# Optimization experiments

Measured on AMD Instinct MI355X. Metric: run time of the kernel, lower is better.

## Reference

```python
import jax, jax.numpy as jnp
import numpy as np

DIM = 768
HEADS = 12
HIDDEN = 3072  # int(dim * 4.0)
EPS = 1e-5


def layernorm(x, g, b):
    mu = jnp.mean(x, axis=-1, keepdims=True)
    var = jnp.mean(jnp.square(x - mu), axis=-1, keepdims=True)
    return (x - mu) * jax.lax.rsqrt(var + EPS) * g + b


def setup_inputs() -> dict:
    key = jax.random.key(0)
    ks = jax.random.split(key, 8)
    s = 0.02
    return {
        "x": jax.random.normal(ks[0], (16, 1024, DIM), dtype=jnp.float32),
        "ln1_g": jnp.ones((DIM,), jnp.float32),
        "ln1_b": jnp.zeros((DIM,), jnp.float32),
        "qkv_w": jax.random.normal(ks[1], (3 * DIM, DIM), jnp.float32) * s,  # torch Linear weight [out,in], no bias (qkv_bias=False)
        "proj_w": jax.random.normal(ks[2], (DIM, DIM), jnp.float32) * s,
        "proj_b": jnp.zeros((DIM,), jnp.float32),
        "ln2_g": jnp.ones((DIM,), jnp.float32),
        "ln2_b": jnp.zeros((DIM,), jnp.float32),
        "fc1_w": jax.random.normal(ks[3], (HIDDEN, DIM), jnp.float32) * s,
        "fc1_b": jnp.zeros((HIDDEN,), jnp.float32),
        "fc2_w": jax.random.normal(ks[4], (DIM, HIDDEN), jnp.float32) * s,
        "fc2_b": jnp.zeros((DIM,), jnp.float32),
    }


def block(x, ln1_g, ln1_b, qkv_w, proj_w, proj_b, ln2_g, ln2_b, fc1_w, fc1_b, fc2_w, fc2_b):
    B, N, C = x.shape
    hd = C // HEADS
    scale = hd ** -0.5
    # --- attention branch ---
    h = layernorm(x, ln1_g, ln1_b)
    qkv = h @ qkv_w.T                                   # [B,N,3C]
    qkv = qkv.reshape(B, N, 3, HEADS, hd)
    q, k, v = jnp.moveaxis(qkv, 2, 0)                   # each [B,N,H,hd]
    q = q.transpose(0, 2, 1, 3)                          # [B,H,N,hd]
    k = k.transpose(0, 2, 1, 3)
    v = v.transpose(0, 2, 1, 3)
    attn = jnp.einsum('bhqd,bhkd->bhqk', q, k) * scale   # [B,H,N,N]
    attn = jax.nn.softmax(attn, axis=-1)
    o = jnp.einsum('bhqk,bhkd->bhqd', attn, v)           # [B,H,N,hd]
    o = o.transpose(0, 2, 1, 3).reshape(B, N, C)
    x = x + o @ proj_w.T + proj_b
    # --- mlp branch ---
    h = layernorm(x, ln2_g, ln2_b)
    h = jax.nn.gelu(h @ fc1_w.T + fc1_b, approximate=False)
    x = x + h @ fc2_w.T + fc2_b
    return x


def reference(x, ln1_g, ln1_b, qkv_w, proj_w, proj_b, ln2_g, ln2_b, fc1_w, fc1_b, fc2_w, fc2_b):
    return block(x, ln1_g, ln1_b, qkv_w, proj_w, proj_b, ln2_g, ln2_b, fc1_w, fc1_b, fc2_w, fc2_b)
```

## Files before the change

kernel.cpp:

```cpp
#include <hip/hip_runtime.h>
#include <cstdint>
#include <cstddef>

typedef __attribute__((ext_vector_type(8))) short short8;
typedef __attribute__((ext_vector_type(4))) float f32x4;
typedef __attribute__((ext_vector_type(4))) unsigned short us4;

#define GAS(p) ((const __attribute__((address_space(1))) void*)(p))
#define LAS(p) ((__attribute__((address_space(3))) void*)(p))

__device__ __forceinline__ unsigned short f2bf(float f) {
  union { float f; unsigned u; } v; v.f = f;
  return (unsigned short)((v.u + 0x7fffu + ((v.u >> 16) & 1u)) >> 16);
}

__global__ __launch_bounds__(256) void cvt_kernel(const float* __restrict__ in,
                                                  unsigned short* __restrict__ out, int n4) {
  int i = blockIdx.x * 256 + threadIdx.x;
  if (i >= n4) return;
  f32x4 v = ((const f32x4*)in)[i];
  us4 o;
#pragma unroll
  for (int j = 0; j < 4; ++j) o[j] = f2bf(v[j]);
  ((us4*)out)[i] = o;
}

__global__ __launch_bounds__(256) void ln_kernel(const float* __restrict__ x,
                                                 const float* __restrict__ g,
                                                 const float* __restrict__ b,
                                                 unsigned short* __restrict__ out) {
  const int wave = threadIdx.x >> 6, lane = threadIdx.x & 63;
  const int row = blockIdx.x * 4 + wave;
  const float* xr = x + (size_t)row * 768;
  f32x4 v[3];
  float s = 0.f, sq = 0.f;
#pragma unroll
  for (int c = 0; c < 3; ++c) {
    v[c] = *(const f32x4*)(xr + c * 256 + lane * 4);
#pragma unroll
    for (int j = 0; j < 4; ++j) { s += v[c][j]; sq += v[c][j] * v[c][j]; }
  }
#pragma unroll
  for (int off = 32; off > 0; off >>= 1) { s += __shfl_xor(s, off); sq += __shfl_xor(sq, off); }
  const float mu = s * (1.f / 768.f);
  const float var = sq * (1.f / 768.f) - mu * mu;
  const float rs = rsqrtf(var + 1e-5f);
  unsigned short* orow = out + (size_t)row * 768;
#pragma unroll
  for (int c = 0; c < 3; ++c) {
    f32x4 gg = *(const f32x4*)(g + c * 256 + lane * 4);
    f32x4 bb = *(const f32x4*)(b + c * 256 + lane * 4);
    us4 o;
#pragma unroll
    for (int j = 0; j < 4; ++j) o[j] = f2bf((v[c][j] - mu) * rs * gg[j] + bb[j]);
    *(us4*)(orow + c * 256 + lane * 4) = o;
  }
}

template <int EPI, int NN, int K>
__global__ __launch_bounds__(1024, 4) void gemmW(
    const unsigned short* __restrict__ A, const unsigned short* __restrict__ W,
    float* __restrict__ outF, const float* __restrict__ bias, const float* __restrict__ res,
    unsigned short* __restrict__ outU,
    unsigned short* __restrict__ q, unsigned short* __restrict__ kk, unsigned short* __restrict__ vt) {
  __shared__ unsigned short As[4][8192];
  __shared__ unsigned short Bs[4][8192];
  const int tid = threadIdx.x;
  const int wave = tid >> 6, lane = tid & 63;
  const int lr = lane & 15, lg = lane >> 4;
  const int wr = wave >> 2, wc = wave & 3;
  constexpr int GX = NN / 256;
  constexpr int NWG = GX * 64;
  int id = blockIdx.y * GX + blockIdx.x;
  id = (id & 7) * (NWG / 8) + (id >> 3);
  const int row0 = (id / GX) * 256, col0 = (id % GX) * 256;
  f32x4 acc[4][4] = {};
  const int sc = ((tid & 3) ^ ((tid >> 3) & 3)) * 8;
  const unsigned short* ag = A + (size_t)(row0 + (tid >> 2)) * K + sc;
  const unsigned short* bg = W + (size_t)(col0 + (tid >> 2)) * K + sc;
  const int rsw = (lg ^ ((lr >> 1) & 3)) << 4;
  constexpr int KT = K / 32;

#define STG(buf, t_)                                                                           \
  {                                                                                            \
    __builtin_amdgcn_global_load_lds(GAS(ag + (t_) * 32), LAS(&As[buf][wave * 512]), 16, 0, 0);\
    __builtin_amdgcn_global_load_lds(GAS(bg + (t_) * 32), LAS(&Bs[buf][wave * 512]), 16, 0, 0);\
  }

#define TILE(buf, t_)                                                                          \
  {                                                                                            \
    if ((t_) < KT - 2)       { asm volatile("s_waitcnt vmcnt(4)" ::: "memory"); }              \
    else if ((t_) == KT - 2) { asm volatile("s_waitcnt vmcnt(2)" ::: "memory"); }              \
    else                     { asm volatile("s_waitcnt vmcnt(0)" ::: "memory"); }              \
    __builtin_amdgcn_s_barrier();                                                              \
    if ((t_) + 3 < KT) STG(((buf) + 3) & 3, (t_) + 3);                                         \
    const char* Ab = (const char*)As + (buf) * 16384;                                          \
    const char* Bb = (const char*)Bs + (buf) * 16384;                                          \
    short8 af[4], bfv[4];                                                                      \
    _Pragma("unroll")                                                                          \
    for (int m = 0; m < 4; ++m) {                                                              \
      const int arow = wr * 64 + m * 16 + lr;                                                  \
      af[m] = *(const short8*)(Ab + arow * 64 + rsw);                                          \
    }                                                                                          \
    _Pragma("unroll")                                                                          \
    for (int n = 0; n < 4; ++n) {                                                              \
      const int brow = wc * 64 + n * 16 + lr;                                                  \
      bfv[n] = *(const short8*)(Bb + brow * 64 + rsw);                                         \
    }                                                                                          \
    __builtin_amdgcn_s_setprio(1);                                                             \
    _Pragma("unroll")                                                                          \
    for (int m = 0; m < 4; ++m)                                                                \
      _Pragma("unroll")                                                                        \
      for (int n = 0; n < 4; ++n)                                                              \
        acc[m][n] = __builtin_amdgcn_mfma_f32_16x16x32_bf16(af[m], bfv[n], acc[m][n], 0, 0, 0);\
    __builtin_amdgcn_s_setprio(0);                                                             \
  }

  STG(0, 0);
  STG(1, 1);
  STG(2, 2);
  for (int tt = 0; tt < KT; tt += 4) {
    TILE(0, tt);
    TILE(1, tt + 1);
    TILE(2, tt + 2);
    TILE(3, tt + 3);
  }
#undef TILE
#undef STG

  if (EPI == 0) {
    const int s = (col0 >= 1536) ? 2 : (col0 >= 768 ? 1 : 0);
    const int hh = (col0 + wc * 64 - s * 768) >> 6;
#pragma unroll
    for (int m = 0; m < 4; ++m)
#pragma unroll
      for (int n = 0; n < 4; ++n) {
        const int d = n * 16 + lr;
        const int g0 = row0 + wr * 64 + m * 16 + lg * 4;
        const int bt = g0 >> 10, nt0 = g0 & 1023;
        const size_t bh = (size_t)(bt * 12 + hh);
        if (s == 2) {
          us4 o;
#pragma unroll
          for (int r = 0; r < 4; ++r) o[r] = f2bf(acc[m][n][r]);
          *(us4*)(vt + (bh * 64 + d) * 1024 + nt0) = o;
        } else {
#pragma unroll
          for (int r = 0; r < 4; ++r) {
            const float val = acc[m][n][r];
            if (s == 0) q[(bh * 1024 + nt0 + r) * 64 + d] = f2bf(val * 0.125f);
            else        kk[(bh * 1024 + nt0 + r) * 64 + d] = f2bf(val);
          }
        }
      }
  } else if (EPI == 1) {
#pragma unroll
    for (int m = 0; m < 4; ++m)
#pragma unroll
      for (int n = 0; n < 4; ++n) {
        const int gcol = col0 + wc * 64 + n * 16 + lr;
        const float bn = bias[gcol];
#pragma unroll
        for (int r = 0; r < 4; ++r) {
          const int grow = row0 + wr * 64 + m * 16 + lg * 4 + r;
          const size_t idx = (size_t)grow * NN + gcol;
          outF[idx] = acc[m][n][r] + bn + res[idx];
        }
      }
  } else {
#pragma unroll
    for (int m = 0; m < 4; ++m)
#pragma unroll
      for (int n = 0; n < 4; ++n) {
        const int gcol = col0 + wc * 64 + n * 16 + lr;
        const float bn = bias[gcol];
#pragma unroll
        for (int r = 0; r < 4; ++r) {
          const int grow = row0 + wr * 64 + m * 16 + lg * 4 + r;
          const size_t idx = (size_t)grow * NN + gcol;
          const float t = acc[m][n][r] + bn;
          const float u = t * (1.59576912f + t * t * 0.07135481f);
          const float eu = __expf(-u);
          outU[idx] = f2bf(t / (1.f + eu));
        }
      }
  }
}

__global__ __launch_bounds__(256) void attn_kernel(
    const unsigned short* __restrict__ Q, const unsigned short* __restrict__ K,
    const unsigned short* __restrict__ V, unsigned short* __restrict__ O) {
  __shared__ unsigned short Ks[2][64 * 64];
  __shared__ unsigned short Vs[2][64 * 64];
  const int tid = threadIdx.x, wave = tid >> 6, lane = tid & 63;
  const int lr = lane & 15, lg = lane >> 4;
  const int id = blockIdx.x;
  const int qt = (id >> 3) & 7;
  const int head = (id & 7) + 8 * (id >> 6);
  const int hh = head % 12, bb = head / 12;
  const size_t bh = (size_t)bb * 12 + hh;
  const unsigned short* Qg = Q + bh * 1024 * 64;
  const unsigned short* Kg = K + bh * 1024 * 64;
  const unsigned short* Vg = V + bh * 64 * 1024;
  const int q0 = qt * 128 + wave * 32;
  short8 aq[2][2];
#pragma unroll
  for (int nq = 0; nq < 2; ++nq)
#pragma unroll
    for (int kb = 0; kb < 2; ++kb)
      aq[nq][kb] = *(const short8*)(Qg + (size_t)(q0 + nq * 16 + lr) * 64 + kb * 32 + lg * 8);
  float m_run[2] = {-1e30f, -1e30f}, l_run[2] = {0.f, 0.f};
  f32x4 oacc[4][2] = {};
  const int srow = tid >> 3;
  const int sswz = (((tid & 7) * 16) ^ ((srow & 7) << 4)) >> 1;
  const int srcLo = (lane & 15) | ((lane & 16) << 1);
  const int srcHi = srcLo + 16;
  const bool hiSel = lg >= 2;

#define ATTN_STAGE(buf, t_)                                                                      \
  {                                                                                              \
    const int kv_ = (t_) * 64;                                                                   \
    _Pragma("unroll")                                                                            \
    for (int is = 0; is < 2; ++is) {                                                             \
      __builtin_amdgcn_global_load_lds(GAS(Kg + (size_t)(kv_ + is * 32 + srow) * 64 + sswz),     \
                                       LAS(&Ks[buf][is * 2048 + wave * 512]), 16, 0, 0);         \
      __builtin_amdgcn_global_load_lds(GAS(Vg + (size_t)(is * 32 + srow) * 1024 + kv_ + sswz),   \
                                       LAS(&Vs[buf][is * 2048 + wave * 512]), 16, 0, 0);         \
    }                                                                                            \
  }

#define ATILE(cur, t_)                                                                           \
  {                                                                                              \
    if ((t_) < 15) { asm volatile("s_waitcnt vmcnt(4)" ::: "memory"); }                          \
    else           { asm volatile("s_waitcnt vmcnt(0)" ::: "memory"); }                          \
    __builtin_amdgcn_s_barrier();                                                                \
    __builtin_amdgcn_sched_barrier(0);                                                           \
    f32x4 sacc[4][2] = {};                                                                       \
    _Pragma("unroll")                                                                            \
    for (int kb = 0; kb < 2; ++kb) {                                                             \
      short8 kf[4];                                                                              \
      _Pragma("unroll")                                                                          \
      for (int mk = 0; mk < 4; ++mk) {                                                           \
        const int row = mk * 16 + lr;                                                            \
        const int boff = row * 128 + ((kb * 64 + lg * 16) ^ ((row & 7) << 4));                   \
        kf[mk] = *(const short8*)((const char*)&Ks[cur][0] + boff);                              \
      }                                                                                          \
      _Pragma("unroll")                                                                          \
      for (int mk = 0; mk < 4; ++mk)                                                             \
        _Pragma("unroll")                                                                        \
        for (int nq = 0; nq < 2; ++nq)                                                           \
          sacc[mk][nq] = __builtin_amdgcn_mfma_f32_16x16x32_bf16(kf[mk], aq[nq][kb], sacc[mk][nq], 0, 0, 0); \
    }                                                                                            \
    unsigned pk[4][2][2];                                                                        \
    _Pragma("unroll")                                                                            \
    for (int nq = 0; nq < 2; ++nq) {                                                             \
      float mx = fmaxf(fmaxf(sacc[0][nq][0], sacc[0][nq][1]), fmaxf(sacc[0][nq][2], sacc[0][nq][3])); \
      _Pragma("unroll")                                                                          \
      for (int mk = 1; mk < 4; ++mk)                                                             \
        mx = fmaxf(mx, fmaxf(fmaxf(sacc[mk][nq][0], sacc[mk][nq][1]), fmaxf(sacc[mk][nq][2], sacc[mk][nq][3]))); \
      mx = fmaxf(mx, __shfl_xor(mx, 16));                                                        \
      mx = fmaxf(mx, __shfl_xor(mx, 32));                                                        \
      if (!__all(mx - m_run[nq] <= 8.f)) {                                                       \
        const float mnew = fmaxf(m_run[nq], mx);                                                 \
        const float alpha = __expf(m_run[nq] - mnew);                                            \
        l_run[nq] *= alpha;                                                                      \
        _Pragma("unroll")                                                                        \
        for (int mb = 0; mb < 4; ++mb)                                                           \
          _Pragma("unroll")                                                                      \
          for (int r = 0; r < 4; ++r) oacc[mb][nq][r] *= alpha;                                  \
        m_run[nq] = mnew;                                                                        \
      }                                                                                          \
      float ssum = 0.f;                                                                          \
      _Pragma("unroll")                                                                          \
      for (int mk = 0; mk < 4; ++mk)                                                             \
        _Pragma("unroll")                                                                        \
        for (int r = 0; r < 4; ++r) {                                                            \
          const float p = __expf(sacc[mk][nq][r] - m_run[nq]);                                   \
          sacc[mk][nq][r] = p;                                                                   \
          ssum += p;                                                                             \
        }                                                                                        \
      ssum += __shfl_xor(ssum, 16);                                                              \
      ssum += __shfl_xor(ssum, 32);                                                              \
      l_run[nq] += ssum;                                                                         \
      _Pragma("unroll")                                                                          \
      for (int mk = 0; mk < 4; ++mk) {                                                           \
        asm("v_cvt_pk_bf16_f32 %0, %1, %2" : "=v"(pk[mk][nq][0]) : "v"(sacc[mk][nq][0]), "v"(sacc[mk][nq][1])); \
        asm("v_cvt_pk_bf16_f32 %0, %1, %2" : "=v"(pk[mk][nq][1]) : "v"(sacc[mk][nq][2]), "v"(sacc[mk][nq][3])); \
      }                                                                                          \
    }                                                                                            \
    _Pragma("unroll")                                                                            \
    for (int kb = 0; kb < 2; ++kb) {                                                             \
      short8 vf[4];                                                                              \
      _Pragma("unroll")                                                                          \
      for (int mb = 0; mb < 4; ++mb) {                                                           \
        const int row = mb * 16 + lr;                                                            \
        const int boff = row * 128 + ((kb * 64 + lg * 16) ^ ((row & 7) << 4));                   \
        vf[mb] = *(const short8*)((const char*)&Vs[cur][0] + boff);                              \
      }                                                                                          \
      _Pragma("unroll")                                                                          \
      for (int nq = 0; nq < 2; ++nq) {                                                           \
        unsigned a0 = (unsigned)__shfl((int)pk[2 * kb][nq][0], srcLo);                           \
        unsigned b0 = (unsigned)__shfl((int)pk[2 * kb + 1][nq][0], srcLo);                       \
        unsigned a1 = (unsigned)__shfl((int)pk[2 * kb][nq][1], srcLo);                           \
        unsigned b1 = (unsigned)__shfl((int)pk[2 * kb + 1][nq][1], srcLo);                       \
        unsigned a2 = (unsigned)__shfl((int)pk[2 * kb][nq][0], srcHi);                           \
        unsigned b2 = (unsigned)__shfl((int)pk[2 * kb + 1][nq][0], srcHi);                       \
        unsigned a3 = (unsigned)__shfl((int)pk[2 * kb][nq][1], srcHi);                           \
        unsigned b3 = (unsigned)__shfl((int)pk[2 * kb + 1][nq][1], srcHi);                       \
        union { unsigned u[4]; short8 s; } cvt;                                                  \
        cvt.u[0] = hiSel ? b0 : a0;                                                              \
        cvt.u[1] = hiSel ? b1 : a1;                                                              \
        cvt.u[2] = hiSel ? b2 : a2;                                                              \
        cvt.u[3] = hiSel ? b3 : a3;                                                              \
        const short8 pb = cvt.s;                                                                 \
        _Pragma("unroll")                                                                        \
        for (int mb = 0; mb < 4; ++mb)                                                           \
          oacc[mb][nq] = __builtin_amdgcn_mfma_f32_16x16x32_bf16(vf[mb], pb, oacc[mb][nq], 0, 0, 0); \
      }                                                                                          \
    }                                                                                            \
    asm volatile("s_waitcnt lgkmcnt(0)" ::: "memory");                                           \
    __builtin_amdgcn_sched_barrier(0);                                                           \
    __builtin_amdgcn_s_barrier();                                                                \
    if ((t_) + 2 < 16) ATTN_STAGE(cur, (t_) + 2);                                                \
  }

  ATTN_STAGE(0, 0);
  ATTN_STAGE(1, 1);
  for (int tt = 0; tt < 8; ++tt) {
    ATILE(0, 2 * tt)
    ATILE(1, 2 * tt + 1)
  }
#undef ATILE
#undef ATTN_STAGE
#pragma unroll
  for (int nq = 0; nq < 2; ++nq) {
    const float linv = 1.f / l_run[nq];
    const size_t tok = (size_t)(bb << 10) + q0 + nq * 16 + lr;
#pragma unroll
    for (int mb = 0; mb < 4; ++mb) {
      us4 o;
#pragma unroll
      for (int r = 0; r < 4; ++r) o[r] = f2bf(oacc[mb][nq][r] * linv);
      *(us4*)(O + tok * 768 + hh * 64 + mb * 16 + lg * 4) = o;
    }
  }
}

extern "C" void kernel_launch(void* const* d_in, const int* in_sizes, int n_in,
                              void* d_out, int out_size, void* d_ws, size_t ws_size,
                              hipStream_t stream) {
  const float* x      = (const float*)d_in[0];
  const float* ln1_g  = (const float*)d_in[1];
  const float* ln1_b  = (const float*)d_in[2];
  const float* qkv_w  = (const float*)d_in[3];
  const float* proj_w = (const float*)d_in[4];
  const float* proj_b = (const float*)d_in[5];
  const float* ln2_g  = (const float*)d_in[6];
  const float* ln2_b  = (const float*)d_in[7];
  const float* fc1_w  = (const float*)d_in[8];
  const float* fc1_b  = (const float*)d_in[9];
  const float* fc2_w  = (const float*)d_in[10];
  const float* fc2_b  = (const float*)d_in[11];
  float* out = (float*)d_out;
  char* ws = (char*)d_ws;

  unsigned short* wqkv = (unsigned short*)(ws + 0);
  unsigned short* wproj = (unsigned short*)(ws + 3538944);
  unsigned short* wfc1 = (unsigned short*)(ws + 4718592);
  unsigned short* wfc2 = (unsigned short*)(ws + 9437184);
  unsigned short* hbuf = (unsigned short*)(ws + 14155776);
  char* big = ws + 39321600;
  unsigned short* qb  = (unsigned short*)(big);
  unsigned short* kb  = (unsigned short*)(big + 25165824);
  unsigned short* vtb = (unsigned short*)(big + 50331648);
  unsigned short* ob  = (unsigned short*)(big + 75497472);
  unsigned short* hid = (unsigned short*)(big);

  cvt_kernel<<<1728, 256, 0, stream>>>(qkv_w, wqkv, 442368);
  cvt_kernel<<<576, 256, 0, stream>>>(proj_w, wproj, 147456);
  cvt_kernel<<<2304, 256, 0, stream>>>(fc1_w, wfc1, 589824);
  cvt_kernel<<<2304, 256, 0, stream>>>(fc2_w, wfc2, 589824);

  ln_kernel<<<4096, 256, 0, stream>>>(x, ln1_g, ln1_b, hbuf);
  gemmW<0, 2304, 768><<<dim3(9, 64), 1024, 0, stream>>>(
      hbuf, wqkv, nullptr, nullptr, nullptr, nullptr, qb, kb, vtb);
  attn_kernel<<<dim3(1536), 256, 0, stream>>>(qb, kb, vtb, ob);
  gemmW<1, 768, 768><<<dim3(3, 64), 1024, 0, stream>>>(
      ob, wproj, out, proj_b, x, nullptr, nullptr, nullptr, nullptr);
  ln_kernel<<<4096, 256, 0, stream>>>(out, ln2_g, ln2_b, hbuf);
  gemmW<2, 3072, 768><<<dim3(12, 64), 1024, 0, stream>>>(
      hbuf, wfc1, nullptr, fc1_b, nullptr, hid, nullptr, nullptr, nullptr);
  gemmW<1, 768, 3072><<<dim3(3, 64), 1024, 0, stream>>>(
      hid, wfc2, out, fc2_b, out, nullptr, nullptr, nullptr, nullptr);
}
```

Before: 472.6 us.

## Stage softmax probabilities through LDS and use exp2 with folded log2e scale

Replaces the eight-shuffle register permutation of the P tile, used to build the MFMA B operand, with a per-wave swizzled LDS buffer: each lane writes its packed bf16 probabilities and reads back the operand layout. It also folds log2(e) into the Q prescale (0.125*1.4427) and switches exp to exp2f, dropping the multiply inside the exponent. This cuts cross-lane shuffle traffic but adds 16KB of shared memory per block, which may lower occupancy. Correctness relies on in-wave ordering of LDS writes before reads with no explicit wait.

New measurement: 462.6 us. -2.1%, faster.

```diff
diff --git a/kernel.cpp b/kernel.cpp
--- a/kernel.cpp
+++ b/kernel.cpp
@@ -148,7 +148,7 @@
 #pragma unroll
           for (int r = 0; r < 4; ++r) {
             const float val = acc[m][n][r];
-            if (s == 0) q[(bh * 1024 + nt0 + r) * 64 + d] = f2bf(val * 0.125f);
+            if (s == 0) q[(bh * 1024 + nt0 + r) * 64 + d] = f2bf(val * 0.18033688f);
             else        kk[(bh * 1024 + nt0 + r) * 64 + d] = f2bf(val);
           }
         }
@@ -192,6 +192,7 @@
     const unsigned short* __restrict__ V, unsigned short* __restrict__ O) {
   __shared__ unsigned short Ks[2][64 * 64];
   __shared__ unsigned short Vs[2][64 * 64];
+  __shared__ unsigned short Ps[4][32 * 64];
   const int tid = threadIdx.x, wave = tid >> 6, lane = tid & 63;
   const int lr = lane & 15, lg = lane >> 4;
   const int id = blockIdx.x;
@@ -213,9 +214,7 @@
   f32x4 oacc[4][2] = {};
   const int srow = tid >> 3;
   const int sswz = (((tid & 7) * 16) ^ ((srow & 7) << 4)) >> 1;
-  const int srcLo = (lane & 15) | ((lane & 16) << 1);
-  const int srcHi = srcLo + 16;
-  const bool hiSel = lg >= 2;
+  char* Pw = (char*)&Ps[wave][0];
 
 #define ATTN_STAGE(buf, t_)                                                                      \
   {                                                                                              \
@@ -251,7 +250,6 @@
         for (int nq = 0; nq < 2; ++nq)                                                           \
           sacc[mk][nq] = __builtin_amdgcn_mfma_f32_16x16x32_bf16(kf[mk], aq[nq][kb], sacc[mk][nq], 0, 0, 0); \
     }                                                                                            \
-    unsigned pk[4][2][2];                                                                        \
     _Pragma("unroll")                                                                            \
     for (int nq = 0; nq < 2; ++nq) {                                                             \
       float mx = fmaxf(fmaxf(sacc[0][nq][0], sacc[0][nq][1]), fmaxf(sacc[0][nq][2], sacc[0][nq][3])); \
@@ -262,7 +260,7 @@
       mx = fmaxf(mx, __shfl_xor(mx, 32));                                                        \
       if (!__all(mx - m_run[nq] <= 8.f)) {                                                       \
         const float mnew = fmaxf(m_run[nq], mx);                                                 \
-        const float alpha = __expf(m_run[nq] - mnew);                                            \
+        const float alpha = exp2f(m_run[nq] - mnew);                                             \
         l_run[nq] *= alpha;                                                                      \
         _Pragma("unroll")                                                                        \
         for (int mb = 0; mb < 4; ++mb)                                                           \
@@ -275,17 +273,21 @@
       for (int mk = 0; mk < 4; ++mk)                                                             \
         _Pragma("unroll")                                                                        \
         for (int r = 0; r < 4; ++r) {                                                            \
-          const float p = __expf(sacc[mk][nq][r] - m_run[nq]);                                   \
+          const float p = exp2f(sacc[mk][nq][r] - m_run[nq]);                                    \
           sacc[mk][nq][r] = p;                                                                   \
           ssum += p;                                                                             \
         }                                                                                        \
       ssum += __shfl_xor(ssum, 16);                                                              \
       ssum += __shfl_xor(ssum, 32);                                                              \
       l_run[nq] += ssum;                                                                         \
+      const int prow = nq * 16 + lr;                                                             \
       _Pragma("unroll")                                                                          \
       for (int mk = 0; mk < 4; ++mk) {                                                           \
-        asm("v_cvt_pk_bf16_f32 %0, %1, %2" : "=v"(pk[mk][nq][0]) : "v"(sacc[mk][nq][0]), "v"(sacc[mk][nq][1])); \
-        asm("v_cvt_pk_bf16_f32 %0, %1, %2" : "=v"(pk[mk][nq][1]) : "v"(sacc[mk][nq][2]), "v"(sacc[mk][nq][3])); \
+        unsigned p0, p1;                                                                         \
+        asm("v_cvt_pk_bf16_f32 %0, %1, %2" : "=v"(p0) : "v"(sacc[mk][nq][0]), "v"(sacc[mk][nq][1])); \
+        asm("v_cvt_pk_bf16_f32 %0, %1, %2" : "=v"(p1) : "v"(sacc[mk][nq][2]), "v"(sacc[mk][nq][3])); \
+        uint2 w; w.x = p0; w.y = p1;                                                             \
+        *(uint2*)(Pw + prow * 128 + ((mk * 32 + lg * 8) ^ ((lr & 7) << 4))) = w;                 \
       }                                                                                          \
     }                                                                                            \
     _Pragma("unroll")                                                                            \
@@ -299,20 +301,8 @@
       }                                                                                          \
       _Pragma("unroll")                                                                          \
       for (int nq = 0; nq < 2; ++nq) {                                                           \
-        unsigned a0 = (unsigned)__shfl((int)pk[2 * kb][nq][0], srcLo);                           \
-        unsigned b0 = (unsigned)__shfl((int)pk[2 * kb + 1][nq][0], srcLo);                       \
-        unsigned a1 = (unsigned)__shfl((int)pk[2 * kb][nq][1], srcLo);                           \
-        unsigned b1 = (unsigned)__shfl((int)pk[2 * kb + 1][nq][1], srcLo);                       \
-        unsigned a2 = (unsigned)__shfl((int)pk[2 * kb][nq][0], srcHi);                           \
-        unsigned b2 = (unsigned)__shfl((int)pk[2 * kb + 1][nq][0], srcHi);                       \
-        unsigned a3 = (unsigned)__shfl((int)pk[2 * kb][nq][1], srcHi);                           \
-        unsigned b3 = (unsigned)__shfl((int)pk[2 * kb + 1][nq][1], srcHi);                       \
-        union { unsigned u[4]; short8 s; } cvt;                                                  \
-        cvt.u[0] = hiSel ? b0 : a0;                                                              \
-        cvt.u[1] = hiSel ? b1 : a1;                                                              \
-        cvt.u[2] = hiSel ? b2 : a2;                                                              \
-        cvt.u[3] = hiSel ? b3 : a3;                                                              \
-        const short8 pb = cvt.s;                                                                 \
+        const int prow = nq * 16 + lr;                                                           \
+        const short8 pb = *(const short8*)(Pw + prow * 128 + ((kb * 64 + lg * 16) ^ ((lr & 7) << 4))); \
         _Pragma("unroll")                                                                        \
         for (int mb = 0; mb < 4; ++mb)                                                           \
           oacc[mb][nq] = __builtin_amdgcn_mfma_f32_16x16x32_bf16(vf[mb], pb, oacc[mb][nq], 0, 0, 0); \
```
